# Optimization experiments

Measured on AMD Instinct MI355X. Metric: run time of the kernel, lower is better.

The kernel has to match this reference:

```python
import jax, jax.numpy as jnp
import numpy as np

B, T, C, H = 2, 2048, 1024, 16
D = C // H  # head dim = 64


def setup_inputs() -> dict:
    key = jax.random.key(0)
    ks = jax.random.split(key, 3)
    x = jax.random.normal(ks[0], (B, T, C), dtype=jnp.float32)
    W_attn = jax.random.normal(ks[1], (C, 3 * C), dtype=jnp.float32) * (1.0 / np.sqrt(C))
    b_attn = jnp.zeros((3 * C,), dtype=jnp.float32)
    W_proj = jax.random.normal(ks[2], (C, C), dtype=jnp.float32) * (1.0 / np.sqrt(C))
    b_proj = jnp.zeros((C,), dtype=jnp.float32)
    return {"x": x, "W_attn": W_attn, "b_attn": b_attn, "W_proj": W_proj, "b_proj": b_proj}


def reference(x, W_attn, b_attn, W_proj, b_proj):
    Bb, Tt, Cc = x.shape
    qkv = x @ W_attn + b_attn                       # [B,T,3C]
    q, k, v = jnp.split(qkv, 3, axis=-1)            # each [B,T,C]
    q = q.reshape(Bb, Tt, H, D).transpose(0, 2, 1, 3)  # [B,H,T,D]
    k = k.reshape(Bb, Tt, H, D).transpose(0, 2, 1, 3)
    v = v.reshape(Bb, Tt, H, D).transpose(0, 2, 1, 3)
    # NOTE: original scales by 1/sqrt(n_embd), not 1/sqrt(head_dim)
    scale = 1.0 / np.sqrt(Cc)
    wei = jnp.einsum('bhqd,bhkd->bhqk', q, k) * scale  # [B,H,T,T]
    causal = jnp.tril(jnp.ones((Tt, Tt), dtype=bool))
    wei = jnp.where(causal, wei, -jnp.inf)
    wei = jax.nn.softmax(wei, axis=-1)
    out = jnp.einsum('bhqk,bhkd->bhqd', wei, v)        # [B,H,T,D]
    out = out.transpose(0, 2, 1, 3).reshape(Bb, Tt, Cc)
    return out @ W_proj + b_proj
```

## Files before the change

### kernel.cpp

```cpp
#include <hip/hip_runtime.h>


typedef short bfrag __attribute__((ext_vector_type(8)));
typedef float facc  __attribute__((ext_vector_type(4)));
typedef float f16v  __attribute__((ext_vector_type(16)));
typedef float f4v   __attribute__((ext_vector_type(4)));
typedef unsigned int u32x2 __attribute__((ext_vector_type(2)));
typedef unsigned int u32x4v __attribute__((ext_vector_type(4)));
typedef unsigned short u16;

#define MFMA16(a, b, c) __builtin_amdgcn_mfma_f32_16x16x32_bf16((a), (b), (c), 0, 0, 0)
#define MFMA32(a, b, c) __builtin_amdgcn_mfma_f32_32x32x16_bf16((a), (b), (c), 0, 0, 0)

__device__ __forceinline__ u16 f2bf(float f) {
  union { float f; unsigned u; } v; v.f = f;
  unsigned r = v.u + 0x7fffu + ((v.u >> 16) & 1u);
  return (u16)(r >> 16);
}

__device__ __forceinline__ unsigned cvtpk(float lo, float hi) {
  unsigned r;
  asm("v_cvt_pk_bf16_f32 %0, %1, %2" : "=v"(r) : "v"(lo), "v"(hi));
  return r;
}

__device__ __forceinline__ void async_lds16(const void* g, void* l) {
  __builtin_amdgcn_global_load_lds(
      (const __attribute__((address_space(1))) unsigned char*)g,
      (__attribute__((address_space(3))) unsigned char*)l, 16, 0, 0);
}


__global__ void cast_bf16_kernel(const float* __restrict__ s, u16* __restrict__ d, int n) {
  int i = (blockIdx.x * blockDim.x + threadIdx.x) * 4;
  if (i >= n) return;
  f4v v = *reinterpret_cast<const f4v*>(s + i);
  u32x2 w;
  w[0] = (unsigned)f2bf(v[0]) | ((unsigned)f2bf(v[1]) << 16);
  w[1] = (unsigned)f2bf(v[2]) | ((unsigned)f2bf(v[3]) << 16);
  *reinterpret_cast<u32x2*>(d + i) = w;
}

__global__ void transpose_cast_kernel(const float* __restrict__ src, u16* __restrict__ dst,
                                      int K, int N) {
  __shared__ float tile[32][33];
  int tx = threadIdx.x, ty = threadIdx.y;
  int n0 = blockIdx.x * 32, k0 = blockIdx.y * 32;
  for (int j = ty; j < 32; j += 8)
    tile[j][tx] = src[(size_t)(k0 + j) * N + (n0 + tx)];
  __syncthreads();
  for (int j = ty; j < 32; j += 8)
    dst[(size_t)(n0 + j) * K + (k0 + tx)] = f2bf(tile[tx][j]);
}


template <int EPI>
__global__ __launch_bounds__(256) void gemm_kernel(
    const u16* __restrict__ A, const u16* __restrict__ Bt,
    const float* __restrict__ bias, float* __restrict__ outf,
    u16* __restrict__ qb, u16* __restrict__ kb, u16* __restrict__ vb) {
  constexpr int KD = 1024;
  __shared__ u16 As[128 * 32];
  __shared__ u16 Bs[128 * 32];
  const int t = threadIdx.x;
  const int l = t & 63, w = t >> 6;
  const int wm = w >> 1, wn = w & 1;
  const int lg = l >> 4, lc = l & 15;
  const int m0 = blockIdx.y * 128, n0 = blockIdx.x * 128;
  facc acc[4][4] = {};
  const int srow = t >> 2, scol = (t & 3) * 8;
  const u16* ga = A + (size_t)(m0 + srow) * KD + scol;
  const u16* gb = Bt + (size_t)(n0 + srow) * KD + scol;
  u16* la0 = As + t * 8;  u16* la1 = As + 2048 + t * 8;
  u16* lb0 = Bs + t * 8;  u16* lb1 = Bs + 2048 + t * 8;
  for (int kt = 0; kt < KD / 32; ++kt) {
    __syncthreads();
    async_lds16(ga + kt * 32, la0);
    async_lds16(ga + 64 * KD + kt * 32, la1);
    async_lds16(gb + kt * 32, lb0);
    async_lds16(gb + 64 * KD + kt * 32, lb1);
    __syncthreads();
    bfrag a[4], b[4];
#pragma unroll
    for (int mi = 0; mi < 4; ++mi)
      a[mi] = *reinterpret_cast<const bfrag*>(As + (wm * 64 + mi * 16 + lc) * 32 + lg * 8);
#pragma unroll
    for (int ni = 0; ni < 4; ++ni)
      b[ni] = *reinterpret_cast<const bfrag*>(Bs + (wn * 64 + ni * 16 + lc) * 32 + lg * 8);
#pragma unroll
    for (int mi = 0; mi < 4; ++mi)
#pragma unroll
      for (int ni = 0; ni < 4; ++ni)
        acc[mi][ni] = MFMA16(a[mi], b[ni], acc[mi][ni]);
  }
#pragma unroll
  for (int mi = 0; mi < 4; ++mi) {
#pragma unroll
    for (int ni = 0; ni < 4; ++ni) {
#pragma unroll
      for (int r = 0; r < 4; ++r) {
        int gm = m0 + wm * 64 + mi * 16 + lg * 4 + r;
        int gn = n0 + wn * 64 + ni * 16 + lc;
        float val = acc[mi][ni][r] + bias[gn];
        if constexpr (EPI == 0) {
          int sec = gn >> 10, ci = gn & 1023;
          int h = ci >> 6, d = ci & 63;
          int b_ = gm >> 11, tq = gm & 2047;
          int bh = b_ * 16 + h;
          if (sec == 0) {
            qb[((size_t)bh * 2048 + tq) * 64 + d] = f2bf(val * 0.045084439f);
          } else if (sec == 1) {
            kb[((size_t)bh * 2048 + tq) * 64 + d] = f2bf(val);
          } else {
            vb[((size_t)bh * 64 + d) * 2048 + tq] = f2bf(val);
          }
        } else {
          outf[(size_t)gm * 1024 + gn] = val;
        }
      }
    }
  }
}


__global__ __launch_bounds__(128, 2) void attn_kernel(
    const u16* __restrict__ Qb, const u16* __restrict__ Kb,
    const u16* __restrict__ Vtb, u16* __restrict__ attn) {
  constexpr int T = 2048;
  __shared__ u16 Ks[2][64 * 64];
  __shared__ u16 Vs[2][64 * 64];
  const int t = threadIdx.x;
  const int l = t & 63, w = t >> 6;
  const int c = l & 31, h = l >> 5;
  const int b = blockIdx.x;
  const int bh = b & 31;
  const int tile = 31 - (b >> 5);
  const int ntile = tile + 1;
  const size_t base = (size_t)bh * T * 64;
  const u16* Qp = Qb + base;
  const u16* Kp = Kb + base;
  const u16* Vp = Vtb + base;
  const int q0 = tile * 64 + w * 32;

  bfrag qf[4];
#pragma unroll
  for (int dt = 0; dt < 4; ++dt)
    qf[dt] = *reinterpret_cast<const bfrag*>(Qp + (size_t)(q0 + c) * 64 + dt * 16 + 8 * h);

  f16v o[2] = {};
  float m_ = -1e30f, l_ = 0.f;

  const int srow = w * 32 + ((l & 63) >> 3);
  const int sw8  = ((t & 7) ^ ((t >> 3) & 7)) * 8;
  const int loff = w * 2048 + l * 8;

#define STAGE(bufi, kvb_)                                                        \
  {                                                                              \
    _Pragma("unroll")                                                            \
    for (int j = 0; j < 4; ++j) {                                                \
      async_lds16(Kp + (size_t)((kvb_) + srow + 8 * j) * 64 + sw8,               \
                  &Ks[bufi][loff + 512 * j]);                                    \
      async_lds16(Vp + (size_t)(srow + 8 * j) * T + (kvb_) + sw8,                \
                  &Vs[bufi][loff + 512 * j]);                                    \
    }                                                                            \
  }

  STAGE(0, 0);
  __syncthreads();

  for (int it = 0; it < ntile; ++it) {
    const int cur = it & 1;
    if (it + 1 < ntile) STAGE(cur ^ 1, 64 * (it + 1));
    const u16* ks = Ks[cur];
    const u16* vs = Vs[cur];

    f16v s[2] = {};
#pragma unroll
    for (int kt = 0; kt < 2; ++kt)
#pragma unroll
      for (int dt = 0; dt < 4; ++dt) {
        const bfrag a = *reinterpret_cast<const bfrag*>(
            ks + (32 * kt + c) * 64 + (((2 * dt + h) ^ (c & 7)) * 8));
        s[kt] = MFMA32(a, qf[dt], s[kt]);
      }

    if (it == ntile - 1) {
      const int kvb = 64 * it;
      const int qq = q0 + c;
#pragma unroll
      for (int kt = 0; kt < 2; ++kt)
#pragma unroll
        for (int r = 0; r < 16; ++r) {
          const int kk = kvb + 32 * kt + (r & 3) + 8 * (r >> 2) + 4 * h;
          if (kk > qq) s[kt][r] = -1e30f;
        }
    }

    {
      float pm = -1e30f;
#pragma unroll
      for (int kt = 0; kt < 2; ++kt)
#pragma unroll
        for (int r = 0; r < 16; ++r) pm = fmaxf(pm, s[kt][r]);
      pm = fmaxf(pm, __shfl_xor(pm, 32));
      if (!__all(pm <= m_ + 8.0f)) {
        const float mn = fmaxf(m_, pm);
        const float al = exp2f(m_ - mn);
        l_ *= al;
#pragma unroll
        for (int r = 0; r < 16; ++r) {
          const float ar = __shfl(al, (r & 3) + 8 * (r >> 2) + 4 * h);
          o[0][r] *= ar;
          o[1][r] *= ar;
        }
        m_ = mn;
      }
      float ps = 0.f;
#pragma unroll
      for (int kt = 0; kt < 2; ++kt)
#pragma unroll
        for (int r = 0; r < 16; ++r) {
          const float e = exp2f(s[kt][r] - m_);
          s[kt][r] = e;
          ps += e;
        }
      ps += __shfl_xor(ps, 32);
      l_ += ps;
    }

    bfrag pa[4];
#pragma unroll
    for (int kt = 0; kt < 2; ++kt)
#pragma unroll
      for (int sub = 0; sub < 2; ++sub) {
        const int bs = 8 * sub;
        unsigned x1 = cvtpk(s[kt][bs + 0], s[kt][bs + 1]);
        unsigned y1 = cvtpk(s[kt][bs + 4], s[kt][bs + 5]);
        asm volatile("v_permlane32_swap_b32 %0, %1" : "+v"(x1), "+v"(y1));
        unsigned x2 = cvtpk(s[kt][bs + 2], s[kt][bs + 3]);
        unsigned y2 = cvtpk(s[kt][bs + 6], s[kt][bs + 7]);
        asm volatile("v_permlane32_swap_b32 %0, %1" : "+v"(x2), "+v"(y2));
        union { u32x4v wv; bfrag f; } u;
        u.wv[0] = x1; u.wv[1] = x2; u.wv[2] = y1; u.wv[3] = y2;
        pa[2 * kt + sub] = u.f;
      }

#pragma unroll
    for (int nt = 0; nt < 2; ++nt)
#pragma unroll
      for (int k2 = 0; k2 < 4; ++k2) {
        const bfrag bv = *reinterpret_cast<const bfrag*>(
            vs + (32 * nt + c) * 64 + (((2 * k2 + h) ^ (c & 7)) * 8));
        o[nt] = MFMA32(pa[k2], bv, o[nt]);
      }

    __syncthreads();
  }

  const int b_ = bh >> 4, hd = bh & 15;
  const float linv = 1.0f / l_;
#pragma unroll
  for (int r = 0; r < 16; ++r) {
    const int row = (r & 3) + 8 * (r >> 2) + 4 * h;
    const float lr = __shfl(linv, row);
    const int tq = q0 + row;
#pragma unroll
    for (int nt = 0; nt < 2; ++nt) {
      const int col = hd * 64 + 32 * nt + c;
      attn[((size_t)(b_ * T + tq)) * 1024 + col] = f2bf(o[nt][r] * lr);
    }
  }
#undef STAGE
}


extern "C" void kernel_launch(void* const* d_in, const int* in_sizes, int n_in,
                              void* d_out, int out_size, void* d_ws, size_t ws_size,
                              hipStream_t stream) {
  const float* x      = (const float*)d_in[0];
  const float* W_attn = (const float*)d_in[1];
  const float* b_attn = (const float*)d_in[2];
  const float* W_proj = (const float*)d_in[3];
  const float* b_proj = (const float*)d_in[4];
  float* out = (float*)d_out;
  char* ws = (char*)d_ws;
  u16* xb   = (u16*)(ws);
  u16* Wat  = (u16*)(ws + (8u  << 20));
  u16* Wpt  = (u16*)(ws + (14u << 20));
  u16* Qb   = (u16*)(ws + (16u << 20));
  u16* Kb   = (u16*)(ws + (24u << 20));
  u16* Vtb  = (u16*)(ws + (32u << 20));
  u16* attn = (u16*)(ws + (40u << 20));

  cast_bf16_kernel<<<4096, 256, 0, stream>>>(x, xb, 4096 * 1024);
  transpose_cast_kernel<<<dim3(96, 32), dim3(32, 8), 0, stream>>>(W_attn, Wat, 1024, 3072);
  transpose_cast_kernel<<<dim3(32, 32), dim3(32, 8), 0, stream>>>(W_proj, Wpt, 1024, 1024);
  gemm_kernel<0><<<dim3(24, 32), 256, 0, stream>>>(xb, Wat, b_attn, nullptr, Qb, Kb, Vtb);
  attn_kernel<<<1024, 128, 0, stream>>>(Qb, Kb, Vtb, attn);
  gemm_kernel<1><<<dim3(8, 32), 256, 0, stream>>>(attn, Wpt, b_proj, out, nullptr, nullptr, nullptr);
}
```

Measured before the change: 137.7 us.

## Software-pipeline attention: overlap QK of next tile with PV, load V directly to registers

```diff
diff --git a/kernel.cpp b/kernel.cpp
--- a/kernel.cpp
+++ b/kernel.cpp
@@ -128,7 +128,6 @@
     const u16* __restrict__ Vtb, u16* __restrict__ attn) {
   constexpr int T = 2048;
   __shared__ u16 Ks[2][64 * 64];
-  __shared__ u16 Vs[2][64 * 64];
   const int t = threadIdx.x;
   const int l = t & 63, w = t >> 6;
   const int c = l & 31, h = l >> 5;
@@ -148,33 +147,35 @@
     qf[dt] = *reinterpret_cast<const bfrag*>(Qp + (size_t)(q0 + c) * 64 + dt * 16 + 8 * h);
 
   f16v o[2] = {};
+  f16v s[2];
   float m_ = -1e30f, l_ = 0.f;
 
-  const int srow = w * 32 + ((l & 63) >> 3);
+  const int srow = w * 32 + (l >> 3);
   const int sw8  = ((t & 7) ^ ((t >> 3) & 7)) * 8;
   const int loff = w * 2048 + l * 8;
 
-#define STAGE(bufi, kvb_)                                                        \
+#define STAGE_K(bufi, kvb_)                                                      \
   {                                                                              \
     _Pragma("unroll")                                                            \
-    for (int j = 0; j < 4; ++j) {                                                \
+    for (int j = 0; j < 4; ++j)                                                  \
       async_lds16(Kp + (size_t)((kvb_) + srow + 8 * j) * 64 + sw8,               \
                   &Ks[bufi][loff + 512 * j]);                                    \
-      async_lds16(Vp + (size_t)(srow + 8 * j) * T + (kvb_) + sw8,                \
-                  &Vs[bufi][loff + 512 * j]);                                    \
-    }                                                                            \
-  }
-
-  STAGE(0, 0);
-  __syncthreads();
-
-  for (int it = 0; it < ntile; ++it) {
-    const int cur = it & 1;
-    if (it + 1 < ntile) STAGE(cur ^ 1, 64 * (it + 1));
-    const u16* ks = Ks[cur];
-    const u16* vs = Vs[cur];
-
-    f16v s[2] = {};
+  }
+
+#define LOADV(vf, kvb_)                                                          \
+  {                                                                              \
+    _Pragma("unroll")                                                            \
+    for (int nt = 0; nt < 2; ++nt)                                               \
+      _Pragma("unroll")                                                          \
+      for (int k2 = 0; k2 < 4; ++k2)                                             \
+        vf[nt * 4 + k2] = *reinterpret_cast<const bfrag*>(                       \
+            Vp + (size_t)(32 * nt + c) * T + (kvb_) + 16 * k2 + 8 * h);          \
+  }
+
+  auto qk = [&](const u16* ks) {
+    const f16v z = {};
+    s[0] = z; s[1] = z;
+    __builtin_amdgcn_s_setprio(1);
 #pragma unroll
     for (int kt = 0; kt < 2; ++kt)
 #pragma unroll
@@ -183,7 +184,20 @@
             ks + (32 * kt + c) * 64 + (((2 * dt + h) ^ (c & 7)) * 8));
         s[kt] = MFMA32(a, qf[dt], s[kt]);
       }
-
+    __builtin_amdgcn_s_setprio(0);
+  };
+
+  auto pv = [&](const bfrag pa[4], const bfrag vf[8]) {
+    __builtin_amdgcn_s_setprio(1);
+#pragma unroll
+    for (int nt = 0; nt < 2; ++nt)
+#pragma unroll
+      for (int k2 = 0; k2 < 4; ++k2)
+        o[nt] = MFMA32(pa[k2], vf[nt * 4 + k2], o[nt]);
+    __builtin_amdgcn_s_setprio(0);
+  };
+
+  auto softmax_pa = [&](int it, bfrag pa[4]) {
     if (it == ntile - 1) {
       const int kvb = 64 * it;
       const int qq = q0 + c;
@@ -195,40 +209,37 @@
           if (kk > qq) s[kt][r] = -1e30f;
         }
     }
-
-    {
-      float pm = -1e30f;
-#pragma unroll
-      for (int kt = 0; kt < 2; ++kt)
-#pragma unroll
-        for (int r = 0; r < 16; ++r) pm = fmaxf(pm, s[kt][r]);
-      pm = fmaxf(pm, __shfl_xor(pm, 32));
-      if (!__all(pm <= m_ + 8.0f)) {
-        const float mn = fmaxf(m_, pm);
-        const float al = exp2f(m_ - mn);
-        l_ *= al;
-#pragma unroll
-        for (int r = 0; r < 16; ++r) {
-          const float ar = __shfl(al, (r & 3) + 8 * (r >> 2) + 4 * h);
-          o[0][r] *= ar;
-          o[1][r] *= ar;
-        }
-        m_ = mn;
-      }
-      float ps = 0.f;
-#pragma unroll
-      for (int kt = 0; kt < 2; ++kt)
-#pragma unroll
-        for (int r = 0; r < 16; ++r) {
-          const float e = exp2f(s[kt][r] - m_);
-          s[kt][r] = e;
-          ps += e;
-        }
-      ps += __shfl_xor(ps, 32);
-      l_ += ps;
+    float pms[4] = {-1e30f, -1e30f, -1e30f, -1e30f};
+#pragma unroll
+    for (int kt = 0; kt < 2; ++kt)
+#pragma unroll
+      for (int r = 0; r < 16; ++r) pms[r & 3] = fmaxf(pms[r & 3], s[kt][r]);
+    float pm = fmaxf(fmaxf(pms[0], pms[1]), fmaxf(pms[2], pms[3]));
+    pm = fmaxf(pm, __shfl_xor(pm, 32));
+    if (!__all(pm <= m_ + 8.0f)) {
+      const float mn = fmaxf(m_, pm);
+      const float al = exp2f(m_ - mn);
+      l_ *= al;
+#pragma unroll
+      for (int r = 0; r < 16; ++r) {
+        const float ar = __shfl(al, (r & 3) + 8 * (r >> 2) + 4 * h);
+        o[0][r] *= ar;
+        o[1][r] *= ar;
+      }
+      m_ = mn;
     }
-
-    bfrag pa[4];
+    float ps[4] = {0.f, 0.f, 0.f, 0.f};
+#pragma unroll
+    for (int kt = 0; kt < 2; ++kt)
+#pragma unroll
+      for (int r = 0; r < 16; ++r) {
+        const float e = exp2f(s[kt][r] - m_);
+        s[kt][r] = e;
+        ps[r & 3] += e;
+      }
+    float pss = (ps[0] + ps[1]) + (ps[2] + ps[3]);
+    pss += __shfl_xor(pss, 32);
+    l_ += pss;
 #pragma unroll
     for (int kt = 0; kt < 2; ++kt)
 #pragma unroll
@@ -244,18 +255,36 @@
         u.wv[0] = x1; u.wv[1] = x2; u.wv[2] = y1; u.wv[3] = y2;
         pa[2 * kt + sub] = u.f;
       }
-
-#pragma unroll
-    for (int nt = 0; nt < 2; ++nt)
-#pragma unroll
-      for (int k2 = 0; k2 < 4; ++k2) {
-        const bfrag bv = *reinterpret_cast<const bfrag*>(
-            vs + (32 * nt + c) * 64 + (((2 * k2 + h) ^ (c & 7)) * 8));
-        o[nt] = MFMA32(pa[k2], bv, o[nt]);
-      }
-
+  };
+
+  bfrag vfA[8], vfB[8], paA[4], paB[4];
+
+  STAGE_K(0, 0);
+  LOADV(vfA, 0);
+  __syncthreads();
+  if (ntile > 1) STAGE_K(1, 64);
+  qk(Ks[0]);
+  softmax_pa(0, paA);
+
+  bool lastA = true;
+  for (int it = 1; it < ntile; ) {
     __syncthreads();
-  }
+    if (it + 1 < ntile) STAGE_K((it + 1) & 1, 64 * (it + 1));
+    LOADV(vfB, 64 * it);
+    qk(Ks[it & 1]);
+    pv(paA, vfA);
+    softmax_pa(it, paB);
+    ++it; lastA = false;
+    if (it >= ntile) break;
+    __syncthreads();
+    if (it + 1 < ntile) STAGE_K((it + 1) & 1, 64 * (it + 1));
+    LOADV(vfA, 64 * it);
+    qk(Ks[it & 1]);
+    pv(paB, vfB);
+    softmax_pa(it, paA);
+    ++it; lastA = true;
+  }
+  if (lastA) pv(paA, vfA); else pv(paB, vfB);
 
   const int b_ = bh >> 4, hd = bh & 15;
   const float linv = 1.0f / l_;
@@ -270,7 +299,8 @@
       attn[((size_t)(b_ * T + tq)) * 1024 + col] = f2bf(o[nt][r] * lr);
     }
   }
-#undef STAGE
+#undef STAGE_K
+#undef LOADV
 }
 
 
```

New measurement: 138.8 us. Within noise of the previous version (+0.8%).
